# Kernel tuning notes

Hardware: AMD Instinct MI355X
Metric: run time of the kernel (lower is better)

The kernel has to match this reference:

```python
import jax, jax.numpy as jnp
import numpy as np

B, N, D, H = 8, 1024, 768, 12
HD = D // H  # head_dim = 64


def setup_inputs() -> dict:
    key = jax.random.key(0)
    ks = jax.random.split(key, 7)
    s = 1.0 / np.sqrt(D)  # xavier-ish scale for weights
    return {
        "x1": jax.random.normal(ks[0], (B, N, D), dtype=jnp.float32),
        "x2": jax.random.normal(ks[1], (B, N, D), dtype=jnp.float32),
        "Wq": jax.random.normal(ks[2], (D, D), dtype=jnp.float32) * s,
        "Wk": jax.random.normal(ks[3], (D, D), dtype=jnp.float32) * s,
        "Wv": jax.random.normal(ks[4], (D, D), dtype=jnp.float32) * s,
        "Wo": jax.random.normal(ks[5], (D, D), dtype=jnp.float32) * s,
        "bo": jnp.zeros((D,), dtype=jnp.float32),
    }


def _heads(x):
    # (B, N, D) -> (B, H, N, HD)
    return x.reshape(B, -1, H, HD).transpose(0, 2, 1, 3)


def reference(x1, x2, Wq, Wk, Wv, Wo, bo):
    scale = 1.0 / jnp.sqrt(jnp.asarray(HD, x1.dtype))
    q1 = _heads(x1 @ Wq.T)               # (B,H,N,HD)
    k1 = _heads(x1 @ Wk.T)
    v1 = _heads(x1 @ Wv.T)
    k2 = _heads(x2 @ Wk.T)
    v2 = _heads(x2 @ Wv.T)
    kc = jnp.concatenate([k1, k2], axis=2)   # (B,H,2N,HD)
    vc = jnp.concatenate([v1, v2], axis=2)
    attn = jnp.einsum('bhnd,bhmd->bhnm', q1, kc) * scale  # (B,H,N,2N)
    attn = jax.nn.softmax(attn, axis=-1)
    out = jnp.einsum('bhnm,bhmd->bhnd', attn, vc)          # (B,H,N,HD)
    out = out.transpose(0, 2, 1, 3).reshape(B, N, D)
    return out @ Wo.T + bo
```

## Files before the change

### kernel.cpp

```cpp
#include <hip/hip_runtime.h>


typedef __bf16 bf16x8 __attribute__((ext_vector_type(8)));
typedef float  f32x4  __attribute__((ext_vector_type(4)));
typedef unsigned int u32x4 __attribute__((ext_vector_type(4)));
typedef short  s16x4  __attribute__((ext_vector_type(4)));
typedef short  s16x8  __attribute__((ext_vector_type(8)));

__device__ __forceinline__ unsigned short bf16bits(float f) {
    return __builtin_bit_cast(unsigned short, (__bf16)f);
}
__device__ __forceinline__ unsigned pk2(float a, float b) {
    return (unsigned)bf16bits(a) | ((unsigned)bf16bits(b) << 16);
}
__device__ __forceinline__ bf16x8 asbf(u32x4 v) {
    return __builtin_bit_cast(bf16x8, v);
}
__device__ __forceinline__ float fexp2(float x) {
#if __has_builtin(__builtin_amdgcn_exp2f)
    return __builtin_amdgcn_exp2f(x);
#else
    return exp2f(x);
#endif
}
__device__ __forceinline__ float frcp(float x) {
#if __has_builtin(__builtin_amdgcn_rcpf)
    return __builtin_amdgcn_rcpf(x);
#else
    return 1.0f / x;
#endif
}

#define MFMA16(a, b, c) __builtin_amdgcn_mfma_f32_16x16x16bf16_1k((a), (b), (c), 0, 0, 0)

__global__ __launch_bounds__(256) void convert_all(
    const float* __restrict__ x1, const float* __restrict__ x2,
    const float* __restrict__ Wq, const float* __restrict__ Wk,
    const float* __restrict__ Wv, const float* __restrict__ Wo,
    unsigned short* __restrict__ x1b, unsigned short* __restrict__ x2b,
    unsigned short* __restrict__ Wcat, unsigned short* __restrict__ Wob)
{
    const float* src; unsigned short* dst; int n4;
    switch (blockIdx.y) {
        case 0:  src = x1; dst = x1b;            n4 = 1572864; break;
        case 1:  src = x2; dst = x2b;            n4 = 1572864; break;
        case 2:  src = Wq; dst = Wcat;           n4 = 147456;  break;
        case 3:  src = Wk; dst = Wcat +  589824; n4 = 147456;  break;
        case 4:  src = Wv; dst = Wcat + 1179648; n4 = 147456;  break;
        default: src = Wo; dst = Wob;            n4 = 147456;  break;
    }
    int i = blockIdx.x * 256 + threadIdx.x;
    if (i >= n4) return;
    float4 v = ((const float4*)src)[i];
    unsigned* o32 = (unsigned*)(dst + (size_t)i * 4);
    o32[0] = pk2(v.x, v.y);
    o32[1] = pk2(v.z, v.w);
}

template<int MODE>
__global__ __launch_bounds__(256) void gemm_qkv(
    const unsigned short* __restrict__ A1, const unsigned short* __restrict__ A2,
    const unsigned short* __restrict__ Wcat,
    unsigned short* __restrict__ dQ, unsigned short* __restrict__ dK,
    unsigned short* __restrict__ dV, float* __restrict__ dO,
    const float* __restrict__ bias)
{
    __shared__ u32x4 smA[1024];
    __shared__ u32x4 smB[1024];

    const int tid  = threadIdx.x;
    const int lane = tid & 63;
    const int l15  = lane & 15;
    const int g    = lane >> 4;
    const int wid  = tid >> 6;
    const int rb   = blockIdx.x;
    const int jb   = blockIdx.y;
    const int wr   = (wid >> 1) * 64;
    const int wc   = (wid & 1) * 64;

    const bool br2 = (MODE == 0) && (jb >= 18);
    const unsigned short* A  = br2 ? A2 : A1;
    const unsigned short* Bw = br2 ? (Wcat + 589824) : Wcat;
    const int jcol = br2 ? (jb - 18) : jb;

    f32x4 acc[4][4] = {};

    for (int kt = 0; kt < 12; ++kt) {
        __syncthreads();
#pragma unroll
        for (int c_ = 0; c_ < 4; ++c_) {
            int i_   = (wid + c_ * 4) * 64 + lane;
            int row_ = i_ >> 3;
            int gs_  = (i_ & 7) ^ (row_ & 7);
            const unsigned short* sa = A +
                (size_t)(rb * 128 + row_) * 768 + kt * 64 + gs_ * 8;
            __builtin_amdgcn_global_load_lds(
                (const __attribute__((address_space(1))) void*)sa,
                (__attribute__((address_space(3))) void*)(smA + (wid + c_ * 4) * 64),
                16, 0, 0);
            const unsigned short* sb = Bw +
                (size_t)(jcol * 128 + row_) * 768 + kt * 64 + gs_ * 8;
            __builtin_amdgcn_global_load_lds(
                (const __attribute__((address_space(1))) void*)sb,
                (__attribute__((address_space(3))) void*)(smB + (wid + c_ * 4) * 64),
                16, 0, 0);
        }
        asm volatile("s_waitcnt vmcnt(0)" ::: "memory");
        __syncthreads();
        __builtin_amdgcn_sched_barrier(0);

#pragma unroll
        for (int kk = 0; kk < 2; ++kk) {
            bf16x8 af[4], bfr[4];
#pragma unroll
            for (int m = 0; m < 4; ++m) {
                int row = wr + m * 16 + l15;
                af[m] = asbf(smA[row * 8 + ((kk * 4 + g) ^ (row & 7))]);
            }
#pragma unroll
            for (int n = 0; n < 4; ++n) {
                int row = wc + n * 16 + l15;
                bfr[n] = asbf(smB[row * 8 + ((kk * 4 + g) ^ (row & 7))]);
            }
#pragma unroll
            for (int m = 0; m < 4; ++m)
#pragma unroll
                for (int n = 0; n < 4; ++n)
                    acc[m][n] = __builtin_amdgcn_mfma_f32_16x16x32_bf16(
                        af[m], bfr[n], acc[m][n], 0, 0, 0);
        }
    }

    const int rloc = wr + g * 4;
    const int cloc = wc + l15;
    const int seg  = jcol / 6;
#pragma unroll
    for (int m = 0; m < 4; ++m) {
#pragma unroll
        for (int n = 0; n < 4; ++n) {
            int r0 = rb * 128 + rloc + m * 16;
            int c  = jcol * 128 + cloc + n * 16;
            if constexpr (MODE == 2) {
#pragma unroll
                for (int reg = 0; reg < 4; ++reg)
                    dO[(size_t)(r0 + reg) * 768 + c] = acc[m][n][reg] + bias[c];
            } else {
                int b = r0 >> 10, nn = r0 & 1023;
                int cl = c - seg * 768;
                int h = cl >> 6, hd = cl & 63;
                int segq = br2 ? seg + 3 : seg;
                if (segq == 0) {
#pragma unroll
                    for (int reg = 0; reg < 4; ++reg)
                        dQ[((size_t)(b * 12 + h) * 1024 + nn + reg) * 64 + hd] =
                            bf16bits(acc[m][n][reg] * 0.18033688f);
                } else if (segq == 1 || segq == 3) {
                    size_t koff = (segq == 3) ? 1024 : 0;
#pragma unroll
                    for (int reg = 0; reg < 4; ++reg)
                        dK[((size_t)(b * 12 + h) * 2048 + koff + nn + reg) * 64 + hd] =
                            bf16bits(acc[m][n][reg]);
                } else {
                    size_t koff = (segq == 4) ? 1024 : 0;
                    int kv = (int)koff + nn;
                    int tt = kv >> 6, u = kv & 63;
                    int up = ((u & 12) << 2) | ((u & 48) >> 2) | (u & 3);
                    uint2 w;
                    w.x = pk2(acc[m][n][0], acc[m][n][1]);
                    w.y = pk2(acc[m][n][2], acc[m][n][3]);
                    *(uint2*)(dV + ((size_t)(b * 12 + h) * 64 + hd) * 2048 +
                              tt * 64 + up) = w;
                }
            }
        }
    }
}

__global__ __launch_bounds__(256, 3) void attn_k(
    const unsigned short* __restrict__ Q, const unsigned short* __restrict__ K,
    const unsigned short* __restrict__ Vt, unsigned short* __restrict__ AO)
{
    __shared__ u32x4 sK[1536];
    __shared__ u32x4 sV[1536];

    const int tid  = threadIdx.x;
    const int lane = tid & 63;
    const int g    = lane >> 4;
    const int l15  = lane & 15;
    const int wid  = tid >> 6;
    const int bh   = blockIdx.x;
    const int q0   = blockIdx.y * 128;

    const unsigned short* Qh = Q  + (size_t)bh * (1024 * 64);
    const unsigned short* Kh = K  + (size_t)bh * (2048 * 64);
    const unsigned short* Vh = Vt + (size_t)bh * (64 * 2048);

    bf16x8 qf[2][2];
#pragma unroll
    for (int m = 0; m < 2; ++m)
#pragma unroll
        for (int kk = 0; kk < 2; ++kk)
            qf[m][kk] = *(const bf16x8*)(Qh +
                (size_t)(q0 + wid * 32 + m * 16 + l15) * 64 + kk * 32 + g * 8);

    f32x4 o[4][2] = {};
    float lr0 = 0.f, lr1 = 0.f;

#define STAGE_TILE(T, DOFF)                                                          \
    {                                                                                \
        int t_ = (T);                                                                \
        _Pragma("unroll")                                                            \
        for (int c_ = 0; c_ < 2; ++c_) {                                             \
            int i_   = (wid + c_ * 4) * 64 + lane;                                   \
            int row_ = i_ >> 3;                                                      \
            int gs_  = (i_ & 7) ^ (row_ & 7);                                        \
            const unsigned short* srcK_ = Kh + ((size_t)t_ * 64 + row_) * 64 + gs_ * 8; \
            __builtin_amdgcn_global_load_lds(                                        \
                (const __attribute__((address_space(1))) void*)srcK_,               \
                (__attribute__((address_space(3))) void*)(sK + (DOFF) + (wid + c_ * 4) * 64), \
                16, 0, 0);                                                           \
            const unsigned short* srcV_ = Vh + (size_t)row_ * 2048 + t_ * 64 + gs_ * 8; \
            __builtin_amdgcn_global_load_lds(                                        \
                (const __attribute__((address_space(1))) void*)srcV_,               \
                (__attribute__((address_space(3))) void*)(sV + (DOFF) + (wid + c_ * 4) * 64), \
                16, 0, 0);                                                           \
        }                                                                            \
    }

    STAGE_TILE(0, 0)
    STAGE_TILE(1, 512)

    for (int t = 0; t < 32; ++t) {
        if (t < 31) { asm volatile("s_waitcnt vmcnt(4)" ::: "memory"); }
        else        { asm volatile("s_waitcnt vmcnt(0)" ::: "memory"); }
        __builtin_amdgcn_s_barrier();
        if (t < 30) {
            STAGE_TILE(t + 2, ((t + 2) % 3) * 512)
        }
        __builtin_amdgcn_sched_barrier(0);

        const u32x4* sKb = sK + (t % 3) * 512;
        const u32x4* sVb = sV + (t % 3) * 512;

        f32x4 s[4][2] = {};
        __builtin_amdgcn_s_setprio(1);
#pragma unroll
        for (int kk = 0; kk < 2; ++kk) {
            bf16x8 kf[4];
#pragma unroll
            for (int n = 0; n < 4; ++n) {
                int row = n * 16 + l15;
                kf[n] = asbf(sKb[row * 8 + ((kk * 4 + g) ^ (row & 7))]);
            }
#pragma unroll
            for (int n = 0; n < 4; ++n)
#pragma unroll
                for (int m = 0; m < 2; ++m)
                    s[n][m] = __builtin_amdgcn_mfma_f32_16x16x32_bf16(
                        kf[n], qf[m][kk], s[n][m], 0, 0, 0);
        }
        __builtin_amdgcn_s_setprio(0);

        float sum0 = 0.f, sum1 = 0.f;
        s16x4 p16[4][2];
#pragma unroll
        for (int n = 0; n < 4; ++n) {
            float p00 = fexp2(s[n][0][0]), p01 = fexp2(s[n][0][1]);
            float p02 = fexp2(s[n][0][2]), p03 = fexp2(s[n][0][3]);
            float p10 = fexp2(s[n][1][0]), p11 = fexp2(s[n][1][1]);
            float p12 = fexp2(s[n][1][2]), p13 = fexp2(s[n][1][3]);
            sum0 += (p00 + p01) + (p02 + p03);
            sum1 += (p10 + p11) + (p12 + p13);
            p16[n][0] = (s16x4){ (short)bf16bits(p00), (short)bf16bits(p01),
                                 (short)bf16bits(p02), (short)bf16bits(p03) };
            p16[n][1] = (s16x4){ (short)bf16bits(p10), (short)bf16bits(p11),
                                 (short)bf16bits(p12), (short)bf16bits(p13) };
        }
        lr0 += sum0; lr1 += sum1;

        __builtin_amdgcn_s_setprio(1);
#pragma unroll
        for (int v = 0; v < 4; ++v) {
            int row = v * 16 + l15;
            int rho = row & 7;
#pragma unroll
            for (int hb = 0; hb < 2; ++hb) {
                s16x8 vv = __builtin_bit_cast(s16x8,
                    sVb[row * 8 + ((2 * g + hb) ^ rho)]);
                s16x4 lo = __builtin_shufflevector(vv, vv, 0, 1, 2, 3);
                s16x4 hi = __builtin_shufflevector(vv, vv, 4, 5, 6, 7);
#pragma unroll
                for (int m = 0; m < 2; ++m)
                    o[v][m] = MFMA16(lo, p16[2 * hb][m], o[v][m]);
#pragma unroll
                for (int m = 0; m < 2; ++m)
                    o[v][m] = MFMA16(hi, p16[2 * hb + 1][m], o[v][m]);
            }
        }
        __builtin_amdgcn_s_setprio(0);
    }

    lr0 += __shfl_xor(lr0, 16); lr0 += __shfl_xor(lr0, 32);
    lr1 += __shfl_xor(lr1, 16); lr1 += __shfl_xor(lr1, 32);
    const int b = bh / 12, h = bh % 12;
    float rl0 = frcp(lr0), rl1 = frcp(lr1);
#pragma unroll
    for (int m = 0; m < 2; ++m) {
        float rl = m ? rl1 : rl0;
        int q = q0 + wid * 32 + m * 16 + l15;
        unsigned short* dst = AO + (size_t)(b * 1024 + q) * 768 + h * 64 + g * 4;
#pragma unroll
        for (int v = 0; v < 4; ++v) {
            uint2 w;
            w.x = pk2(o[v][m][0] * rl, o[v][m][1] * rl);
            w.y = pk2(o[v][m][2] * rl, o[v][m][3] * rl);
            *(uint2*)(dst + v * 16) = w;
        }
    }
#undef STAGE_TILE
}

extern "C" void kernel_launch(void* const* d_in, const int* in_sizes, int n_in,
                              void* d_out, int out_size, void* d_ws, size_t ws_size,
                              hipStream_t stream)
{
    const float* x1 = (const float*)d_in[0];
    const float* x2 = (const float*)d_in[1];
    const float* Wq = (const float*)d_in[2];
    const float* Wk = (const float*)d_in[3];
    const float* Wv = (const float*)d_in[4];
    const float* Wo = (const float*)d_in[5];
    const float* bo = (const float*)d_in[6];

    unsigned short* Wcat = (unsigned short*)d_ws;
    unsigned short* Wob  = Wcat + 1769472;
    unsigned short* x1b  = Wob  + 589824;
    unsigned short* x2b  = x1b  + 6291456;
    unsigned short* Qb   = x2b  + 6291456;
    unsigned short* Kc   = Qb   + 6291456;
    unsigned short* Vt   = Kc   + 12582912;
    unsigned short* AO   = x1b;

    convert_all<<<dim3(6144, 6), 256, 0, stream>>>(x1, x2, Wq, Wk, Wv, Wo,
                                                   x1b, x2b, Wcat, Wob);

    gemm_qkv<0><<<dim3(64, 30), 256, 0, stream>>>(x1b, x2b, Wcat,
                                                  Qb, Kc, Vt, nullptr, nullptr);

    attn_k<<<dim3(96, 8), 256, 0, stream>>>(Qb, Kc, Vt, AO);

    gemm_qkv<2><<<dim3(64, 6), 256, 0, stream>>>(AO, nullptr, Wob,
                                                 nullptr, nullptr, nullptr,
                                                 (float*)d_out, bo);
}
```

Measured before the change: 174.1 us.

## Double-buffer QKV GEMM loads and use 16x16x32 MFMA for PV product

The QKV/output GEMM now double-buffers its LDS tiles, so the global-to-LDS loads for the next k-tile are issued before computing the current one instead of stalling on vmcnt(0) each iteration. The attention kernel's P·V product switches from 16x16x16 MFMAs to 16x16x32 MFMAs. To make this work, the K rows in LDS are permuted so the score accumulator layout lines up with the wider PV operand, and V is stored in plain order instead of the previous interleaved layout. This doubles GEMM shared memory, which may lower occupancy, and relies on the new K row permutation and swizzle being consistent.

Result: faster. 159.7 us (-8.3%).

```diff
diff --git a/kernel.cpp b/kernel.cpp
--- a/kernel.cpp
+++ b/kernel.cpp
@@ -31,7 +31,7 @@
 #endif
 }
 
-#define MFMA16(a, b, c) __builtin_amdgcn_mfma_f32_16x16x16bf16_1k((a), (b), (c), 0, 0, 0)
+#define MFMA32(a, b, c) __builtin_amdgcn_mfma_f32_16x16x32_bf16((a), (b), (c), 0, 0, 0)
 
 __global__ __launch_bounds__(256) void convert_all(
     const float* __restrict__ x1, const float* __restrict__ x2,
@@ -65,8 +65,8 @@
     unsigned short* __restrict__ dV, float* __restrict__ dO,
     const float* __restrict__ bias)
 {
-    __shared__ u32x4 smA[1024];
-    __shared__ u32x4 smB[1024];
+    __shared__ u32x4 smA[2048];
+    __shared__ u32x4 smB[2048];
 
     const int tid  = threadIdx.x;
     const int lane = tid & 63;
@@ -85,29 +85,44 @@
 
     f32x4 acc[4][4] = {};
 
+#define GSTAGE(KT, BO)                                                               \
+    {                                                                                \
+        int kt_ = (KT);                                                              \
+        _Pragma("unroll")                                                            \
+        for (int c_ = 0; c_ < 4; ++c_) {                                             \
+            int i_   = (wid + c_ * 4) * 64 + lane;                                   \
+            int row_ = i_ >> 3;                                                      \
+            int gs_  = (i_ & 7) ^ (row_ & 7);                                        \
+            const unsigned short* sa = A +                                           \
+                (size_t)(rb * 128 + row_) * 768 + kt_ * 64 + gs_ * 8;                \
+            __builtin_amdgcn_global_load_lds(                                        \
+                (const __attribute__((address_space(1))) void*)sa,                   \
+                (__attribute__((address_space(3))) void*)(smA + (BO) + (wid + c_ * 4) * 64), \
+                16, 0, 0);                                                           \
+            const unsigned short* sb = Bw +                                          \
+                (size_t)(jcol * 128 + row_) * 768 + kt_ * 64 + gs_ * 8;              \
+            __builtin_amdgcn_global_load_lds(                                        \
+                (const __attribute__((address_space(1))) void*)sb,                   \
+                (__attribute__((address_space(3))) void*)(smB + (BO) + (wid + c_ * 4) * 64), \
+                16, 0, 0);                                                           \
+        }                                                                            \
+    }
+
+    GSTAGE(0, 0)
+
     for (int kt = 0; kt < 12; ++kt) {
-        __syncthreads();
-#pragma unroll
-        for (int c_ = 0; c_ < 4; ++c_) {
-            int i_   = (wid + c_ * 4) * 64 + lane;
-            int row_ = i_ >> 3;
-            int gs_  = (i_ & 7) ^ (row_ & 7);
-            const unsigned short* sa = A +
-                (size_t)(rb * 128 + row_) * 768 + kt * 64 + gs_ * 8;
-            __builtin_amdgcn_global_load_lds(
-                (const __attribute__((address_space(1))) void*)sa,
-                (__attribute__((address_space(3))) void*)(smA + (wid + c_ * 4) * 64),
-                16, 0, 0);
-            const unsigned short* sb = Bw +
-                (size_t)(jcol * 128 + row_) * 768 + kt * 64 + gs_ * 8;
-            __builtin_amdgcn_global_load_lds(
-                (const __attribute__((address_space(1))) void*)sb,
-                (__attribute__((address_space(3))) void*)(smB + (wid + c_ * 4) * 64),
-                16, 0, 0);
-        }
-        asm volatile("s_waitcnt vmcnt(0)" ::: "memory");
-        __syncthreads();
+        __builtin_amdgcn_s_barrier();
+        if (kt < 11) {
+            GSTAGE(kt + 1, ((kt + 1) & 1) << 10)
+            asm volatile("s_waitcnt vmcnt(8)" ::: "memory");
+        } else {
+            asm volatile("s_waitcnt vmcnt(0)" ::: "memory");
+        }
+        __builtin_amdgcn_s_barrier();
         __builtin_amdgcn_sched_barrier(0);
+
+        const u32x4* bA = smA + ((kt & 1) << 10);
+        const u32x4* bB = smB + ((kt & 1) << 10);
 
 #pragma unroll
         for (int kk = 0; kk < 2; ++kk) {
@@ -115,21 +130,21 @@
 #pragma unroll
             for (int m = 0; m < 4; ++m) {
                 int row = wr + m * 16 + l15;
-                af[m] = asbf(smA[row * 8 + ((kk * 4 + g) ^ (row & 7))]);
+                af[m] = asbf(bA[row * 8 + ((kk * 4 + g) ^ (row & 7))]);
             }
 #pragma unroll
             for (int n = 0; n < 4; ++n) {
                 int row = wc + n * 16 + l15;
-                bfr[n] = asbf(smB[row * 8 + ((kk * 4 + g) ^ (row & 7))]);
+                bfr[n] = asbf(bB[row * 8 + ((kk * 4 + g) ^ (row & 7))]);
             }
 #pragma unroll
             for (int m = 0; m < 4; ++m)
 #pragma unroll
                 for (int n = 0; n < 4; ++n)
-                    acc[m][n] = __builtin_amdgcn_mfma_f32_16x16x32_bf16(
-                        af[m], bfr[n], acc[m][n], 0, 0, 0);
-        }
-    }
+                    acc[m][n] = MFMA32(af[m], bfr[n], acc[m][n]);
+        }
+    }
+#undef GSTAGE
 
     const int rloc = wr + g * 4;
     const int cloc = wc + l15;
@@ -162,14 +177,11 @@
                             bf16bits(acc[m][n][reg]);
                 } else {
                     size_t koff = (segq == 4) ? 1024 : 0;
-                    int kv = (int)koff + nn;
-                    int tt = kv >> 6, u = kv & 63;
-                    int up = ((u & 12) << 2) | ((u & 48) >> 2) | (u & 3);
                     uint2 w;
                     w.x = pk2(acc[m][n][0], acc[m][n][1]);
                     w.y = pk2(acc[m][n][2], acc[m][n][3]);
                     *(uint2*)(dV + ((size_t)(b * 12 + h) * 64 + hd) * 2048 +
-                              tt * 64 + up) = w;
+                              koff + nn) = w;
                 }
             }
         }
@@ -213,13 +225,14 @@
         for (int c_ = 0; c_ < 2; ++c_) {                                             \
             int i_   = (wid + c_ * 4) * 64 + lane;                                   \
             int row_ = i_ >> 3;                                                      \
-            int gs_  = (i_ & 7) ^ (row_ & 7);                                        \
-            const unsigned short* srcK_ = Kh + ((size_t)t_ * 64 + row_) * 64 + gs_ * 8; \
+            int gsK_ = (i_ & 7) ^ ((row_ & 3) | ((row_ >> 1) & 4));                  \
+            int gsV_ = (i_ & 7) ^ (row_ & 7);                                        \
+            const unsigned short* srcK_ = Kh + ((size_t)t_ * 64 + row_) * 64 + gsK_ * 8; \
             __builtin_amdgcn_global_load_lds(                                        \
                 (const __attribute__((address_space(1))) void*)srcK_,               \
                 (__attribute__((address_space(3))) void*)(sK + (DOFF) + (wid + c_ * 4) * 64), \
                 16, 0, 0);                                                           \
-            const unsigned short* srcV_ = Vh + (size_t)row_ * 2048 + t_ * 64 + gs_ * 8; \
+            const unsigned short* srcV_ = Vh + (size_t)row_ * 2048 + t_ * 64 + gsV_ * 8; \
             __builtin_amdgcn_global_load_lds(                                        \
                 (const __attribute__((address_space(1))) void*)srcV_,               \
                 (__attribute__((address_space(3))) void*)(sV + (DOFF) + (wid + c_ * 4) * 64), \
@@ -249,15 +262,15 @@
             bf16x8 kf[4];
 #pragma unroll
             for (int n = 0; n < 4; ++n) {
-                int row = n * 16 + l15;
-                kf[n] = asbf(sKb[row * 8 + ((kk * 4 + g) ^ (row & 7))]);
+                int rowp = ((n & 1) << 5) + ((l15 >> 2) << 3) +
+                           (((n >> 1) & 1) << 2) + (l15 & 3);
+                kf[n] = asbf(sKb[rowp * 8 + ((kk * 4 + g) ^ (l15 & 7))]);
             }
 #pragma unroll
             for (int n = 0; n < 4; ++n)
 #pragma unroll
                 for (int m = 0; m < 2; ++m)
-                    s[n][m] = __builtin_amdgcn_mfma_f32_16x16x32_bf16(
-                        kf[n], qf[m][kk], s[n][m], 0, 0, 0);
+                    s[n][m] = MFMA32(kf[n], qf[m][kk], s[n][m]);
         }
         __builtin_amdgcn_s_setprio(0);
 
@@ -280,21 +293,20 @@
 
         __builtin_amdgcn_s_setprio(1);
 #pragma unroll
-        for (int v = 0; v < 4; ++v) {
-            int row = v * 16 + l15;
-            int rho = row & 7;
-#pragma unroll
-            for (int hb = 0; hb < 2; ++hb) {
-                s16x8 vv = __builtin_bit_cast(s16x8,
-                    sVb[row * 8 + ((2 * g + hb) ^ rho)]);
-                s16x4 lo = __builtin_shufflevector(vv, vv, 0, 1, 2, 3);
-                s16x4 hi = __builtin_shufflevector(vv, vv, 4, 5, 6, 7);
+        for (int kk = 0; kk < 2; ++kk) {
+            bf16x8 pf[2];
+#pragma unroll
+            for (int m = 0; m < 2; ++m)
+                pf[m] = __builtin_bit_cast(bf16x8,
+                    __builtin_shufflevector(p16[kk][m], p16[kk + 2][m],
+                                            0, 1, 2, 3, 4, 5, 6, 7));
+#pragma unroll
+            for (int v = 0; v < 4; ++v) {
+                int row = v * 16 + l15;
+                bf16x8 vf = asbf(sVb[row * 8 + ((kk * 4 + g) ^ (row & 7))]);
 #pragma unroll
                 for (int m = 0; m < 2; ++m)
-                    o[v][m] = MFMA16(lo, p16[2 * hb][m], o[v][m]);
-#pragma unroll
-                for (int m = 0; m < 2; ++m)
-                    o[v][m] = MFMA16(hi, p16[2 * hb + 1][m], o[v][m]);
+                    o[v][m] = MFMA32(vf, pf[m], o[v][m]);
             }
         }
         __builtin_amdgcn_s_setprio(0);
```
